# Kernel tuning notes

Measured on AMD Instinct MI355X. Metric: run time of the kernel, lower is better.

The kernel has to match this reference:

```python
import jax, jax.numpy as jnp
import numpy as np

N, F_IN, H = 8192, 128, 256
AVG_DEG_P = 16.0 / N  # ~16 neighbors per node, BA-graph-like sparsity


def setup_inputs() -> dict:
    key = jax.random.key(0)
    ks = jax.random.split(key, 16)
    # symmetric 0/1 adjacency, no self-loops
    B = jax.random.bernoulli(ks[0], AVG_DEG_P, (N, N)).astype(jnp.float32)
    A = jnp.maximum(B, B.T)
    A = A * (1.0 - jnp.eye(N, dtype=jnp.float32))
    features = jax.random.normal(ks[1], (N, F_IN), dtype=jnp.float32)
    treatments = jax.random.bernoulli(ks[2], 0.1, (N, 1)).astype(jnp.float32)
    def glorot(k, shape):
        lim = float(np.sqrt(6.0 / (shape[0] + shape[1])))
        return jax.random.uniform(k, shape, jnp.float32, -lim, lim)
    return {
        "A": A,
        "features": features,
        "treatments": treatments,
        "W1": glorot(ks[3], (F_IN, H)),   # GCNConv layer 1 weight
        "b1": jnp.zeros((H,), jnp.float32),
        "W2": glorot(ks[4], (H, H)),      # GCNConv layer 2 weight
        "b2": jnp.zeros((H,), jnp.float32),
        "W_emb": glorot(ks[5], (H + 1, H)),
        "b_emb": jnp.zeros((H,), jnp.float32),
        "W_t0": glorot(ks[6], (H, 1)),
        "b_t0": jnp.zeros((1,), jnp.float32),
        "W_t1": glorot(ks[7], (H, 1)),
        "b_t1": jnp.zeros((1,), jnp.float32),
    }


def _gcn_norm(A):
    # PyG GCNConv default: D^-1/2 (A + I) D^-1/2
    A_hat = A + jnp.eye(A.shape[0], dtype=A.dtype)
    d = jnp.sum(A_hat, axis=1)
    dinv = jnp.where(d > 0, 1.0 / jnp.sqrt(d), 0.0)
    return A_hat * dinv[:, None] * dinv[None, :]


def reference(A, features, treatments, W1, b1, W2, b2, W_emb, b_emb, W_t0, b_t0, W_t1, b_t1):
    nA = _gcn_norm(A)                                  # [N, N]
    h = jax.nn.relu(nA @ (features @ W1) + b1)         # GCNConv 1, [N, H]
    h = jax.nn.relu(nA @ (h @ W2) + b2)                # GCNConv 2, [N, H]
    deg = jnp.sum(A, axis=1) + 1e-8                    # [N]
    # faithful to torch: (A * treatments).sum(dim=1) broadcasts treatments[N,1] over columns
    exposure = (jnp.sum(A * treatments, axis=1) / deg)[:, None]  # [N, 1]
    rep = jnp.concatenate([h, exposure], axis=1)       # [N, H+1]
    emb = jax.nn.relu(rep @ W_emb + b_emb)             # [N, H]
    y0_pred = (emb @ W_t0 + b_t0).reshape(-1)          # [N]
    y1_pred = (emb @ W_t1 + b_t1).reshape(-1)          # [N]
    return (y0_pred, y1_pred, emb)
```

## Files before the change

### kernel.cpp

```cpp
#include <hip/hip_runtime.h>

#define NN   8192
#define FIN  128
#define HH   256
#define CAP  128

typedef float    f32x4 __attribute__((ext_vector_type(4)));
typedef float    f32x2 __attribute__((ext_vector_type(2)));
typedef _Float16 f16x8 __attribute__((ext_vector_type(8)));
typedef _Float16 f16x4 __attribute__((ext_vector_type(4)));
typedef _Float16 f16x2 __attribute__((ext_vector_type(2)));

__device__ __forceinline__ const f32x4* c4(const float* p) { return (const f32x4*)p; }
__device__ __forceinline__       f32x4* p4(float* p)       { return (f32x4*)p; }
__device__ __forceinline__ const f32x2* c2(const float* p) { return (const f32x2*)p; }
__device__ __forceinline__       f32x2* p2(float* p)       { return (f32x2*)p; }

__global__ __launch_bounds__(256) void k_build(
    const float* __restrict__ A, const float* __restrict__ treat,
    const float* __restrict__ X,
    const float* __restrict__ W2, const float* __restrict__ W_emb,
    int* __restrict__ cols, int* __restrict__ cnt,
    float* __restrict__ dinv, float* __restrict__ expo,
    _Float16* __restrict__ Xh, _Float16* __restrict__ W2T,
    _Float16* __restrict__ WembT)
{
  const int row = blockIdx.x;
  if (row >= NN) {
    const int q = row - NN;
    if (q < 128) {
      const int t0 = q * 256 + threadIdx.x;
      for (int i = t0; i < NN * FIN / 4; i += 128 * 256) {
        const f32x4 v = *c4(&X[(size_t)i * 4]);
        f16x4 h = {(_Float16)v[0], (_Float16)v[1], (_Float16)v[2], (_Float16)v[3]};
        *(f16x4*)&Xh[(size_t)i * 4] = h;
      }
    } else if (q < 132) {
      for (int e = (q - 128) * 256 + threadIdx.x; e < HH * HH; e += 1024) {
        const int k = e >> 8, n = e & 255;
        W2T[(size_t)n * HH + k] = (_Float16)W2[e];
      }
    } else {
      for (int e = (q - 132) * 256 + threadIdx.x; e < HH * HH; e += 1024) {
        const int k = e >> 8, n = e & 255;
        WembT[(size_t)n * HH + k] = (_Float16)W_emb[e];
      }
    }
    return;
  }

  const f32x4* Ar = c4(A + (size_t)row * NN);
  __shared__ int   s_cnt;
  __shared__ float s_rs[4];
  if (threadIdx.x == 0) s_cnt = 0;
  __syncthreads();

  float rs = 0.f;
  int* myCols = cols + (size_t)row * CAP;
  #pragma unroll
  for (int it = 0; it < NN / 4 / 256; ++it) {
    const int idx = it * 256 + threadIdx.x;
    const f32x4 a = __builtin_nontemporal_load(Ar + idx);
    const int base = idx * 4;
    #pragma unroll
    for (int u = 0; u < 4; ++u) {
      if (a[u] != 0.0f) {
        rs += a[u];
        int p = atomicAdd(&s_cnt, 1);
        if (p < CAP) myCols[p] = base + u;
      }
    }
  }
  #pragma unroll
  for (int off = 32; off > 0; off >>= 1) rs += __shfl_down(rs, off);
  const int wid = threadIdx.x >> 6;
  if ((threadIdx.x & 63) == 0) s_rs[wid] = rs;
  __syncthreads();
  if (threadIdx.x == 0) {
    const float R = s_rs[0] + s_rs[1] + s_rs[2] + s_rs[3];
    int n = s_cnt; if (n > CAP) n = CAP;
    cnt[row]  = n;
    dinv[row] = rsqrtf(R + 1.0f);
    expo[row] = treat[row] * R / (R + 1e-8f);
  }
}

__global__ __launch_bounds__(256) void k_agg0h(
    const _Float16* __restrict__ Xh,
    const int* __restrict__ cols, const int* __restrict__ cnt,
    const float* __restrict__ dinv, float* __restrict__ out)
{
  const int wid  = threadIdx.x >> 6;
  const int lane = threadIdx.x & 63;
  const int i    = blockIdx.x * 4 + wid;
  __shared__ int   s_cols[4][CAP];
  __shared__ float s_w[4][CAP];

  const int n = cnt[i];
  if (lane < n) {
    const int j = cols[(size_t)i * CAP + lane];
    s_cols[wid][lane] = j;  s_w[wid][lane] = dinv[j];
  }
  if (lane + 64 < n) {
    const int j = cols[(size_t)i * CAP + lane + 64];
    s_cols[wid][lane + 64] = j;  s_w[wid][lane + 64] = dinv[j];
  }
  __syncthreads();

  const float di = dinv[i];
  const f16x2 sv = *(const f16x2*)&Xh[(size_t)i * FIN + 2 * lane];
  f32x2 acc = {di * (float)sv[0], di * (float)sv[1]};
  #pragma unroll 4
  for (int t = 0; t < n; ++t) {
    const int   j = s_cols[wid][t];
    const float w = s_w[wid][t];
    const f16x2 v = *(const f16x2*)&Xh[(size_t)j * FIN + 2 * lane];
    acc[0] += w * (float)v[0];
    acc[1] += w * (float)v[1];
  }
  *p2(&out[(size_t)i * FIN + 2 * lane]) = di * acc;
}

template<bool INIT>
__global__ __launch_bounds__(256) void k_aggh(
    const _Float16* __restrict__ M,
    const int* __restrict__ cols, const int* __restrict__ cnt,
    const float* __restrict__ dinv, const float* __restrict__ bias,
    _Float16* __restrict__ out,
    float* __restrict__ dout, const float* __restrict__ bt0, const float* __restrict__ bt1)
{
  const int wid  = threadIdx.x >> 6;
  const int lane = threadIdx.x & 63;
  const int i    = blockIdx.x * 4 + wid;
  __shared__ int   s_cols[4][CAP];
  __shared__ float s_w[4][CAP];

  if constexpr (INIT) {
    if (blockIdx.x < 64) {
      const int idx = blockIdx.x * 256 + threadIdx.x;
      dout[idx] = (idx < NN) ? bt0[0] : bt1[0];
    }
  }

  const int n = cnt[i];
  if (lane < n) {
    const int j = cols[(size_t)i * CAP + lane];
    s_cols[wid][lane] = j;  s_w[wid][lane] = dinv[j];
  }
  if (lane + 64 < n) {
    const int j = cols[(size_t)i * CAP + lane + 64];
    s_cols[wid][lane + 64] = j;  s_w[wid][lane + 64] = dinv[j];
  }
  __syncthreads();

  const float di = dinv[i];
  const f32x4 bias4 = *c4(&bias[lane * 4]);
  const f16x4 sv = *(const f16x4*)&M[(size_t)i * HH + 4 * lane];
  f32x4 acc = {di * (float)sv[0], di * (float)sv[1],
               di * (float)sv[2], di * (float)sv[3]};
  #pragma unroll 4
  for (int t = 0; t < n; ++t) {
    const int   j = s_cols[wid][t];
    const float w = s_w[wid][t];
    const f16x4 v = *(const f16x4*)&M[(size_t)j * HH + 4 * lane];
    acc[0] += w * (float)v[0];
    acc[1] += w * (float)v[1];
    acc[2] += w * (float)v[2];
    acc[3] += w * (float)v[3];
  }
  f32x4 o = di * acc + bias4;
  f16x4 oh;
  #pragma unroll
  for (int q = 0; q < 4; ++q) oh[q] = (_Float16)fmaxf(o[q], 0.f);
  *(f16x4*)&out[(size_t)i * HH + 4 * lane] = oh;
}

template<bool FIN_EPI>
__global__ __launch_bounds__(256) void k_gemm_mfma(
    const _Float16* __restrict__ Ah, const _Float16* __restrict__ BT,
    const float* __restrict__ Wfull,
    const float* __restrict__ bias, const float* __restrict__ expo,
    const float* __restrict__ Wt0, const float* __restrict__ Wt1,
    float* __restrict__ out, _Float16* __restrict__ out16,
    float* __restrict__ y0, float* __restrict__ y1)
{
  const int tid = threadIdx.x;
  const int w = tid >> 6, l = tid & 63;
  const int r0 = (blockIdx.x & 127) * 64 + w * 16;
  const int c0 = (blockIdx.x >> 7) * 64;
  const int lr = l & 15;
  const int lk = (l >> 4) * 8;

  f32x4 acc[4] = {{0.f,0.f,0.f,0.f},{0.f,0.f,0.f,0.f},
                  {0.f,0.f,0.f,0.f},{0.f,0.f,0.f,0.f}};
  const _Float16* Aptr = Ah + (size_t)(r0 + lr) * HH + lk;
  const _Float16* Bptr = BT + (size_t)(c0 + lr) * HH + lk;

  #pragma unroll
  for (int k0 = 0; k0 < HH; k0 += 32) {
    const f16x8 a = *(const f16x8*)(Aptr + k0);
    #pragma unroll
    for (int nt = 0; nt < 4; ++nt) {
      const f16x8 b = *(const f16x8*)(Bptr + (size_t)nt * 16 * HH + k0);
      acc[nt] = __builtin_amdgcn_mfma_f32_16x16x32_f16(a, b, acc[nt], 0, 0, 0);
    }
  }

  const int rbase = r0 + (l >> 4) * 4;
  if constexpr (!FIN_EPI) {
    #pragma unroll
    for (int r = 0; r < 4; ++r)
      #pragma unroll
      for (int nt = 0; nt < 4; ++nt)
        out16[(size_t)(rbase + r) * HH + c0 + 16 * nt + lr] = (_Float16)acc[nt][r];
  } else {
    float eb[4], bs[4], w0[4], w1[4];
    #pragma unroll
    for (int nt = 0; nt < 4; ++nt) {
      const int c = c0 + 16 * nt + lr;
      eb[nt] = Wfull[(size_t)HH * HH + c];
      bs[nt] = bias[c];
      w0[nt] = Wt0[c];
      w1[nt] = Wt1[c];
    }
    #pragma unroll
    for (int r = 0; r < 4; ++r) {
      const int R = rbase + r;
      const float e = expo[R];
      float s0 = 0.f, s1 = 0.f;
      #pragma unroll
      for (int nt = 0; nt < 4; ++nt) {
        float v = fmaxf(acc[nt][r] + e * eb[nt] + bs[nt], 0.f);
        out[(size_t)R * HH + c0 + 16 * nt + lr] = v;
        s0 += v * w0[nt];
        s1 += v * w1[nt];
      }
      #pragma unroll
      for (int off = 8; off > 0; off >>= 1) {
        s0 += __shfl_down(s0, off);
        s1 += __shfl_down(s1, off);
      }
      if (lr == 0) {
        atomicAdd(&y0[R], s0);
        atomicAdd(&y1[R], s1);
      }
    }
  }
}

template<int K>
__global__ __launch_bounds__(256) void k_gemm_v(
    const float* __restrict__ M, const float* __restrict__ W,
    const float* __restrict__ bias, _Float16* __restrict__ out16)
{
  __shared__ float As[16][64];
  __shared__ float Bs[16][64];
  const int tid = threadIdx.x;
  const int tx = tid & 15, ty = tid >> 4;
  const int bx = blockIdx.x & 127, by = blockIdx.x >> 7;
  const int r0 = bx * 64, c0 = by * 64;
  const int la_r = tid & 63;
  const int la_k = (tid >> 6) << 2;
  const int lb_k = tid >> 4;
  const int lb_c = (tid & 15) << 2;

  const float* Abase = M + (size_t)(r0 + la_r) * K + la_k;
  const float* Bbase = W + (size_t)lb_k * HH + c0 + lb_c;

  f32x4 aR = *c4(Abase);
  f32x4 bR = *c4(Bbase);
  float acc[4][4] = {};

  #pragma unroll 1
  for (int k0 = 0; k0 < K; k0 += 16) {
    As[la_k + 0][la_r] = aR[0];
    As[la_k + 1][la_r] = aR[1];
    As[la_k + 2][la_r] = aR[2];
    As[la_k + 3][la_r] = aR[3];
    *p4(&Bs[lb_k][lb_c]) = bR;
    __syncthreads();
    if (k0 + 16 < K) {
      aR = *c4(Abase + k0 + 16);
      bR = *c4(Bbase + (size_t)(k0 + 16) * HH);
    }
    #pragma unroll
    for (int kk = 0; kk < 16; ++kk) {
      const f32x4 av = *c4(&As[kk][ty * 4]);
      const f32x4 bv = *c4(&Bs[kk][tx * 4]);
      #pragma unroll
      for (int i = 0; i < 4; ++i)
        #pragma unroll
        for (int j = 0; j < 4; ++j)
          acc[i][j] += av[i] * bv[j];
    }
    __syncthreads();
  }

  const f32x4 bs = *c4(&bias[c0 + tx * 4]);
  #pragma unroll
  for (int i = 0; i < 4; ++i) {
    const int r = r0 + ty * 4 + i;
    f16x4 oh;
    #pragma unroll
    for (int j = 0; j < 4; ++j) oh[j] = (_Float16)fmaxf(acc[i][j] + bs[j], 0.f);
    *(f16x4*)&out16[(size_t)r * HH + c0 + tx * 4] = oh;
  }
}

extern "C" void kernel_launch(void* const* d_in, const int* in_sizes, int n_in,
                              void* d_out, int out_size, void* d_ws, size_t ws_size,
                              hipStream_t stream)
{
  const float* A      = (const float*)d_in[0];
  const float* feats  = (const float*)d_in[1];
  const float* treat  = (const float*)d_in[2];
  const float* W1     = (const float*)d_in[3];
  const float* b1     = (const float*)d_in[4];
  const float* W2     = (const float*)d_in[5];
  const float* b2     = (const float*)d_in[6];
  const float* W_emb  = (const float*)d_in[7];
  const float* b_emb  = (const float*)d_in[8];
  const float* W_t0   = (const float*)d_in[9];
  const float* b_t0   = (const float*)d_in[10];
  const float* W_t1   = (const float*)d_in[11];
  const float* b_t1   = (const float*)d_in[12];
  float* dout = (float*)d_out;

  int*      cols  = (int*)d_ws;
  int*      cnt   = cols + (size_t)NN * CAP;
  float*    dinv  = (float*)(cnt + NN);
  float*    expo  = dinv + NN;
  float*    bufX  = expo + NN;
  _Float16* Xh    = (_Float16*)(bufX + (size_t)NN * FIN);
  _Float16* h1h   = Xh + (size_t)NN * FIN;
  _Float16* h1w2h = h1h + (size_t)NN * HH;
  _Float16* h2h   = h1w2h + (size_t)NN * HH;
  _Float16* W2T   = h2h + (size_t)NN * HH;
  _Float16* WembT = W2T + (size_t)HH * HH;

  float* y0  = dout;
  float* y1  = dout + NN;
  float* emb = dout + 2 * NN;

  k_build<<<NN + 136, 256, 0, stream>>>(A, treat, feats, W2, W_emb,
                                        cols, cnt, dinv, expo, Xh, W2T, WembT);
  k_agg0h<<<NN / 4, 256, 0, stream>>>(Xh, cols, cnt, dinv, bufX);
  k_gemm_v<FIN><<<512, 256, 0, stream>>>(bufX, W1, b1, h1h);
  k_gemm_mfma<false><<<512, 256, 0, stream>>>(
      h1h, W2T, nullptr, nullptr, nullptr, nullptr, nullptr,
      nullptr, h1w2h, nullptr, nullptr);
  k_aggh<true><<<NN / 4, 256, 0, stream>>>(h1w2h, cols, cnt, dinv, b2, h2h,
                                           dout, b_t0, b_t1);
  k_gemm_mfma<true><<<512, 256, 0, stream>>>(
      h2h, WembT, W_emb, b_emb, expo, W_t0, W_t1,
      emb, nullptr, y0, y1);
}
```

Baseline: 433.9 us.

## Use MFMA for first GCN GEMM and split neighbor loops across half-waves

Replaces the fp32 shared-memory SIMT GEMM for layer 1 with the fp16 MFMA GEMM, templated on K, using a transposed fp16 W1 built in the setup kernel. The aggregated layer-0 features are now stored in fp16. Both aggregation kernels split the neighbor loop between the two half-waves with wider per-lane vectors and combine them with a cross-lane shuffle. Output-bias initialization moves into the build kernel. The cost is fp16 rounding of the aggregated features and some idle lanes in the epilogue.

```diff
diff --git a/kernel.cpp b/kernel.cpp
--- a/kernel.cpp
+++ b/kernel.cpp
@@ -13,17 +13,18 @@
 
 __device__ __forceinline__ const f32x4* c4(const float* p) { return (const f32x4*)p; }
 __device__ __forceinline__       f32x4* p4(float* p)       { return (f32x4*)p; }
-__device__ __forceinline__ const f32x2* c2(const float* p) { return (const f32x2*)p; }
-__device__ __forceinline__       f32x2* p2(float* p)       { return (f32x2*)p; }
 
 __global__ __launch_bounds__(256) void k_build(
     const float* __restrict__ A, const float* __restrict__ treat,
     const float* __restrict__ X,
-    const float* __restrict__ W2, const float* __restrict__ W_emb,
+    const float* __restrict__ W1, const float* __restrict__ W2,
+    const float* __restrict__ W_emb,
+    const float* __restrict__ bt0, const float* __restrict__ bt1,
     int* __restrict__ cols, int* __restrict__ cnt,
     float* __restrict__ dinv, float* __restrict__ expo,
-    _Float16* __restrict__ Xh, _Float16* __restrict__ W2T,
-    _Float16* __restrict__ WembT)
+    _Float16* __restrict__ Xh, _Float16* __restrict__ W1T,
+    _Float16* __restrict__ W2T, _Float16* __restrict__ WembT,
+    float* __restrict__ dout)
 {
   const int row = blockIdx.x;
   if (row >= NN) {
@@ -40,11 +41,20 @@
         const int k = e >> 8, n = e & 255;
         W2T[(size_t)n * HH + k] = (_Float16)W2[e];
       }
-    } else {
+    } else if (q < 136) {
       for (int e = (q - 132) * 256 + threadIdx.x; e < HH * HH; e += 1024) {
         const int k = e >> 8, n = e & 255;
         WembT[(size_t)n * HH + k] = (_Float16)W_emb[e];
       }
+    } else if (q < 138) {
+      for (int e = (q - 136) * 256 + threadIdx.x; e < HH * FIN; e += 512) {
+        const int n = e >> 7, k = e & 127;
+        W1T[e] = (_Float16)W1[(size_t)k * HH + n];
+      }
+    } else {
+      const float v0 = bt0[0], v1 = bt1[0];
+      for (int i = (q - 138) * 256 + threadIdx.x; i < 2 * NN; i += 2048)
+        dout[i] = (i < NN) ? v0 : v1;
     }
     return;
   }
@@ -88,10 +98,12 @@
 __global__ __launch_bounds__(256) void k_agg0h(
     const _Float16* __restrict__ Xh,
     const int* __restrict__ cols, const int* __restrict__ cnt,
-    const float* __restrict__ dinv, float* __restrict__ out)
+    const float* __restrict__ dinv, _Float16* __restrict__ out)
 {
   const int wid  = threadIdx.x >> 6;
   const int lane = threadIdx.x & 63;
+  const int half = lane >> 5;
+  const int cl   = lane & 31;
   const int i    = blockIdx.x * 4 + wid;
   __shared__ int   s_cols[4][CAP];
   __shared__ float s_w[4][CAP];
@@ -108,39 +120,42 @@
   __syncthreads();
 
   const float di = dinv[i];
-  const f16x2 sv = *(const f16x2*)&Xh[(size_t)i * FIN + 2 * lane];
-  f32x2 acc = {di * (float)sv[0], di * (float)sv[1]};
-  #pragma unroll 4
-  for (int t = 0; t < n; ++t) {
+  f32x4 acc = {0.f, 0.f, 0.f, 0.f};
+  if (half == 0) {
+    const f16x4 sv = *(const f16x4*)&Xh[(size_t)i * FIN + 4 * cl];
+    #pragma unroll
+    for (int q = 0; q < 4; ++q) acc[q] = di * (float)sv[q];
+  }
+  for (int t = half; t < n; t += 2) {
     const int   j = s_cols[wid][t];
     const float w = s_w[wid][t];
-    const f16x2 v = *(const f16x2*)&Xh[(size_t)j * FIN + 2 * lane];
-    acc[0] += w * (float)v[0];
-    acc[1] += w * (float)v[1];
-  }
-  *p2(&out[(size_t)i * FIN + 2 * lane]) = di * acc;
-}
-
-template<bool INIT>
+    const f16x4 v = *(const f16x4*)&Xh[(size_t)j * FIN + 4 * cl];
+    #pragma unroll
+    for (int q = 0; q < 4; ++q) acc[q] += w * (float)v[q];
+  }
+  #pragma unroll
+  for (int q = 0; q < 4; ++q) acc[q] += __shfl_xor(acc[q], 32);
+  if (half == 0) {
+    f16x4 oh;
+    #pragma unroll
+    for (int q = 0; q < 4; ++q) oh[q] = (_Float16)(di * acc[q]);
+    *(f16x4*)&out[(size_t)i * FIN + 4 * cl] = oh;
+  }
+}
+
 __global__ __launch_bounds__(256) void k_aggh(
     const _Float16* __restrict__ M,
     const int* __restrict__ cols, const int* __restrict__ cnt,
     const float* __restrict__ dinv, const float* __restrict__ bias,
-    _Float16* __restrict__ out,
-    float* __restrict__ dout, const float* __restrict__ bt0, const float* __restrict__ bt1)
+    _Float16* __restrict__ out)
 {
   const int wid  = threadIdx.x >> 6;
   const int lane = threadIdx.x & 63;
+  const int half = lane >> 5;
+  const int cl   = lane & 31;
   const int i    = blockIdx.x * 4 + wid;
   __shared__ int   s_cols[4][CAP];
   __shared__ float s_w[4][CAP];
-
-  if constexpr (INIT) {
-    if (blockIdx.x < 64) {
-      const int idx = blockIdx.x * 256 + threadIdx.x;
-      dout[idx] = (idx < NN) ? bt0[0] : bt1[0];
-    }
-  }
 
   const int n = cnt[i];
   if (lane < n) {
@@ -154,28 +169,35 @@
   __syncthreads();
 
   const float di = dinv[i];
-  const f32x4 bias4 = *c4(&bias[lane * 4]);
-  const f16x4 sv = *(const f16x4*)&M[(size_t)i * HH + 4 * lane];
-  f32x4 acc = {di * (float)sv[0], di * (float)sv[1],
-               di * (float)sv[2], di * (float)sv[3]};
-  #pragma unroll 4
-  for (int t = 0; t < n; ++t) {
+  float acc[8] = {};
+  if (half == 0) {
+    const f16x8 sv = *(const f16x8*)&M[(size_t)i * HH + 8 * cl];
+    #pragma unroll
+    for (int q = 0; q < 8; ++q) acc[q] = di * (float)sv[q];
+  }
+  for (int t = half; t < n; t += 2) {
     const int   j = s_cols[wid][t];
     const float w = s_w[wid][t];
-    const f16x4 v = *(const f16x4*)&M[(size_t)j * HH + 4 * lane];
-    acc[0] += w * (float)v[0];
-    acc[1] += w * (float)v[1];
-    acc[2] += w * (float)v[2];
-    acc[3] += w * (float)v[3];
-  }
-  f32x4 o = di * acc + bias4;
-  f16x4 oh;
-  #pragma unroll
-  for (int q = 0; q < 4; ++q) oh[q] = (_Float16)fmaxf(o[q], 0.f);
-  *(f16x4*)&out[(size_t)i * HH + 4 * lane] = oh;
-}
-
-template<bool FIN_EPI>
+    const f16x8 v = *(const f16x8*)&M[(size_t)j * HH + 8 * cl];
+    #pragma unroll
+    for (int q = 0; q < 8; ++q) acc[q] += w * (float)v[q];
+  }
+  #pragma unroll
+  for (int q = 0; q < 8; ++q) acc[q] += __shfl_xor(acc[q], 32);
+  if (half == 0) {
+    const f32x4 b0 = *c4(&bias[8 * cl]);
+    const f32x4 b1 = *c4(&bias[8 * cl + 4]);
+    f16x8 oh;
+    #pragma unroll
+    for (int q = 0; q < 4; ++q) {
+      oh[q]     = (_Float16)fmaxf(di * acc[q]     + b0[q], 0.f);
+      oh[q + 4] = (_Float16)fmaxf(di * acc[q + 4] + b1[q], 0.f);
+    }
+    *(f16x8*)&out[(size_t)i * HH + 8 * cl] = oh;
+  }
+}
+
+template<int K, int MODE>
 __global__ __launch_bounds__(256) void k_gemm_mfma(
     const _Float16* __restrict__ Ah, const _Float16* __restrict__ BT,
     const float* __restrict__ Wfull,
@@ -193,26 +215,36 @@
 
   f32x4 acc[4] = {{0.f,0.f,0.f,0.f},{0.f,0.f,0.f,0.f},
                   {0.f,0.f,0.f,0.f},{0.f,0.f,0.f,0.f}};
-  const _Float16* Aptr = Ah + (size_t)(r0 + lr) * HH + lk;
-  const _Float16* Bptr = BT + (size_t)(c0 + lr) * HH + lk;
-
-  #pragma unroll
-  for (int k0 = 0; k0 < HH; k0 += 32) {
+  const _Float16* Aptr = Ah + (size_t)(r0 + lr) * K + lk;
+  const _Float16* Bptr = BT + (size_t)(c0 + lr) * K + lk;
+
+  #pragma unroll
+  for (int k0 = 0; k0 < K; k0 += 32) {
     const f16x8 a = *(const f16x8*)(Aptr + k0);
     #pragma unroll
     for (int nt = 0; nt < 4; ++nt) {
-      const f16x8 b = *(const f16x8*)(Bptr + (size_t)nt * 16 * HH + k0);
+      const f16x8 b = *(const f16x8*)(Bptr + (size_t)nt * 16 * K + k0);
       acc[nt] = __builtin_amdgcn_mfma_f32_16x16x32_f16(a, b, acc[nt], 0, 0, 0);
     }
   }
 
   const int rbase = r0 + (l >> 4) * 4;
-  if constexpr (!FIN_EPI) {
+  if constexpr (MODE == 0) {
     #pragma unroll
     for (int r = 0; r < 4; ++r)
       #pragma unroll
       for (int nt = 0; nt < 4; ++nt)
         out16[(size_t)(rbase + r) * HH + c0 + 16 * nt + lr] = (_Float16)acc[nt][r];
+  } else if constexpr (MODE == 1) {
+    float bs[4];
+    #pragma unroll
+    for (int nt = 0; nt < 4; ++nt) bs[nt] = bias[c0 + 16 * nt + lr];
+    #pragma unroll
+    for (int r = 0; r < 4; ++r)
+      #pragma unroll
+      for (int nt = 0; nt < 4; ++nt)
+        out16[(size_t)(rbase + r) * HH + c0 + 16 * nt + lr] =
+            (_Float16)fmaxf(acc[nt][r] + bs[nt], 0.f);
   } else {
     float eb[4], bs[4], w0[4], w1[4];
     #pragma unroll
@@ -245,65 +277,6 @@
         atomicAdd(&y1[R], s1);
       }
     }
-  }
-}
-
-template<int K>
-__global__ __launch_bounds__(256) void k_gemm_v(
-    const float* __restrict__ M, const float* __restrict__ W,
-    const float* __restrict__ bias, _Float16* __restrict__ out16)
-{
-  __shared__ float As[16][64];
-  __shared__ float Bs[16][64];
-  const int tid = threadIdx.x;
-  const int tx = tid & 15, ty = tid >> 4;
-  const int bx = blockIdx.x & 127, by = blockIdx.x >> 7;
-  const int r0 = bx * 64, c0 = by * 64;
-  const int la_r = tid & 63;
-  const int la_k = (tid >> 6) << 2;
-  const int lb_k = tid >> 4;
-  const int lb_c = (tid & 15) << 2;
-
-  const float* Abase = M + (size_t)(r0 + la_r) * K + la_k;
-  const float* Bbase = W + (size_t)lb_k * HH + c0 + lb_c;
-
-  f32x4 aR = *c4(Abase);
-  f32x4 bR = *c4(Bbase);
-  float acc[4][4] = {};
-
-  #pragma unroll 1
-  for (int k0 = 0; k0 < K; k0 += 16) {
-    As[la_k + 0][la_r] = aR[0];
-    As[la_k + 1][la_r] = aR[1];
-    As[la_k + 2][la_r] = aR[2];
-    As[la_k + 3][la_r] = aR[3];
-    *p4(&Bs[lb_k][lb_c]) = bR;
-    __syncthreads();
-    if (k0 + 16 < K) {
-      aR = *c4(Abase + k0 + 16);
-      bR = *c4(Bbase + (size_t)(k0 + 16) * HH);
-    }
-    #pragma unroll
-    for (int kk = 0; kk < 16; ++kk) {
-      const f32x4 av = *c4(&As[kk][ty * 4]);
-      const f32x4 bv = *c4(&Bs[kk][tx * 4]);
-      #pragma unroll
-      for (int i = 0; i < 4; ++i)
-        #pragma unroll
-        for (int j = 0; j < 4; ++j)
-          acc[i][j] += av[i] * bv[j];
-    }
-    __syncthreads();
-  }
-
-  const f32x4 bs = *c4(&bias[c0 + tx * 4]);
-  #pragma unroll
-  for (int i = 0; i < 4; ++i) {
-    const int r = r0 + ty * 4 + i;
-    f16x4 oh;
-    #pragma unroll
-    for (int j = 0; j < 4; ++j) oh[j] = (_Float16)fmaxf(acc[i][j] + bs[j], 0.f);
-    *(f16x4*)&out16[(size_t)r * HH + c0 + tx * 4] = oh;
   }
 }
 
@@ -330,28 +303,32 @@
   int*      cnt   = cols + (size_t)NN * CAP;
   float*    dinv  = (float*)(cnt + NN);
   float*    expo  = dinv + NN;
-  float*    bufX  = expo + NN;
-  _Float16* Xh    = (_Float16*)(bufX + (size_t)NN * FIN);
-  _Float16* h1h   = Xh + (size_t)NN * FIN;
+  _Float16* Xh    = (_Float16*)(expo + NN);
+  _Float16* aggXh = Xh + (size_t)NN * FIN;
+  _Float16* h1h   = aggXh + (size_t)NN * FIN;
   _Float16* h1w2h = h1h + (size_t)NN * HH;
   _Float16* h2h   = h1w2h + (size_t)NN * HH;
-  _Float16* W2T   = h2h + (size_t)NN * HH;
+  _Float16* W1T   = h2h + (size_t)NN * HH;
+  _Float16* W2T   = W1T + (size_t)HH * FIN;
   _Float16* WembT = W2T + (size_t)HH * HH;
 
   float* y0  = dout;
   float* y1  = dout + NN;
   float* emb = dout + 2 * NN;
 
-  k_build<<<NN + 136, 256, 0, stream>>>(A, treat, feats, W2, W_emb,
-                                        cols, cnt, dinv, expo, Xh, W2T, WembT);
-  k_agg0h<<<NN / 4, 256, 0, stream>>>(Xh, cols, cnt, dinv, bufX);
-  k_gemm_v<FIN><<<512, 256, 0, stream>>>(bufX, W1, b1, h1h);
-  k_gemm_mfma<false><<<512, 256, 0, stream>>>(
+  k_build<<<NN + 146, 256, 0, stream>>>(A, treat, feats, W1, W2, W_emb,
+                                        b_t0, b_t1,
+                                        cols, cnt, dinv, expo,
+                                        Xh, W1T, W2T, WembT, dout);
+  k_agg0h<<<NN / 4, 256, 0, stream>>>(Xh, cols, cnt, dinv, aggXh);
+  k_gemm_mfma<FIN, 1><<<512, 256, 0, stream>>>(
+      aggXh, W1T, nullptr, b1, nullptr, nullptr, nullptr,
+      nullptr, h1h, nullptr, nullptr);
+  k_gemm_mfma<HH, 0><<<512, 256, 0, stream>>>(
       h1h, W2T, nullptr, nullptr, nullptr, nullptr, nullptr,
       nullptr, h1w2h, nullptr, nullptr);
-  k_aggh<true><<<NN / 4, 256, 0, stream>>>(h1w2h, cols, cnt, dinv, b2, h2h,
-                                           dout, b_t0, b_t1);
-  k_gemm_mfma<true><<<512, 256, 0, stream>>>(
+  k_aggh<<<NN / 4, 256, 0, stream>>>(h1w2h, cols, cnt, dinv, b2, h2h);
+  k_gemm_mfma<HH, 2><<<512, 256, 0, stream>>>(
       h2h, WembT, W_emb, b_emb, expo, W_t0, W_t1,
       emb, nullptr, y0, y1);
 }
```

New measurement: 432.6 us. Within noise of the previous version (-0.3%).
